# Performance work log

Hardware: AMD Instinct MI355X
Metric: run time of the kernel (lower is better)

## Reference

```python
import jax, jax.numpy as jnp
import numpy as np

N_HEAD = 16
LOCAL_CTX = 256
W_SCALE = 0.02  # keep logits in a sane range, like trained-net init


def setup_inputs() -> dict:
    key = jax.random.key(0)
    k1, k2, k3 = jax.random.split(key, 3)
    B, T, C = 4, 2048, 1024
    x = jax.random.normal(k1, (B, T, C), dtype=jnp.float32)
    W_attn = jax.random.normal(k2, (C, 3 * C), dtype=jnp.float32) * W_SCALE
    b_attn = jnp.zeros((3 * C,), dtype=jnp.float32)
    W_proj = jax.random.normal(k3, (C, C), dtype=jnp.float32) * W_SCALE
    b_proj = jnp.zeros((C,), dtype=jnp.float32)
    return {"x": x, "W_attn": W_attn, "b_attn": b_attn,
            "W_proj": W_proj, "b_proj": b_proj}


def _local_causal_mask(T, ctx):
    # token i attends to j with j <= i and i - j < ctx  (band of width ctx)
    i = jnp.arange(T)[:, None]
    j = jnp.arange(T)[None, :]
    ctx = min(T, ctx)
    return (j <= i) & ((i - j) < ctx)  # [T, T] bool


def reference(x, W_attn, b_attn, W_proj, b_proj):
    B, T, C = x.shape
    H = N_HEAD
    D = C // H
    qkv = x @ W_attn + b_attn                       # [B, T, 3C]
    q, k, v = jnp.split(qkv, 3, axis=-1)
    q = q.reshape(B, T, H, D).transpose(0, 2, 1, 3)  # [B, H, T, D]
    k = k.reshape(B, T, H, D).transpose(0, 2, 1, 3)
    v = v.reshape(B, T, H, D).transpose(0, 2, 1, 3)
    scale = 1.0 / jnp.sqrt(jnp.asarray(D, dtype=x.dtype))
    w = jnp.einsum('bhtd,bhsd->bhts', q, k) * scale  # [B, H, T, T]
    mask = _local_causal_mask(T, LOCAL_CTX)          # [T, T]
    w = jnp.where(mask[None, None], w, -jnp.inf)
    p = jax.nn.softmax(w, axis=-1)
    a = jnp.einsum('bhts,bhsd->bhtd', p, v)          # [B, H, T, D]
    y = a.transpose(0, 2, 1, 3).reshape(B, T, C)
    return y @ W_proj + b_proj
```

## Files before the change

kernel.cpp:

```cpp
#include <hip/hip_runtime.h>
#include <stdint.h>

#define B_SZ 4
#define T_SEQ 2048
#define C_DIM 1024
#define NH 16
#define DH 64
#define CTX 256

#define AS_G const __attribute__((address_space(1))) void*
#define AS_L __attribute__((address_space(3))) void*

typedef __attribute__((ext_vector_type(8))) short bf16x8;
typedef __attribute__((ext_vector_type(8))) unsigned short u16x8;
typedef __attribute__((ext_vector_type(4))) unsigned short u16x4;
typedef __attribute__((ext_vector_type(2))) unsigned int u32x2;
typedef __attribute__((ext_vector_type(4))) unsigned int u32x4;
typedef __attribute__((ext_vector_type(4))) float f32x4;

__device__ __forceinline__ float bf2f(unsigned short u) {
  unsigned int x = ((unsigned int)u) << 16;
  return __builtin_bit_cast(float, x);
}
__device__ __forceinline__ unsigned short f2bf(float f) {
  unsigned int u = __builtin_bit_cast(unsigned int, f);
  u = (u + 0x7FFFu + ((u >> 16) & 1u)) >> 16;
  return (unsigned short)u;
}
__device__ __forceinline__ unsigned int cvtpk(float lo, float hi) {
  unsigned int r;
  asm("v_cvt_pk_bf16_f32 %0, %1, %2" : "=v"(r) : "v"(lo), "v"(hi));
  return r;
}


__global__ void cvt_f32_bf16(const float* __restrict__ in,
                             unsigned short* __restrict__ out, int n8) {
  int i = blockIdx.x * blockDim.x + threadIdx.x;
  int stride = gridDim.x * blockDim.x;
  for (; i < n8; i += stride) {
    float4 a = ((const float4*)in)[2 * (size_t)i];
    float4 b = ((const float4*)in)[2 * (size_t)i + 1];
    u32x4 r;
    r[0] = cvtpk(a.x, a.y); r[1] = cvtpk(a.z, a.w);
    r[2] = cvtpk(b.x, b.y); r[3] = cvtpk(b.z, b.w);
    *(u32x4*)(out + 8 * (size_t)i) = r;
  }
}

__global__ void transpose_cvt(const float* __restrict__ W,
                              unsigned short* __restrict__ Wt, int R, int CC) {
  __shared__ float tile[32][33];
  int ct = blockIdx.x, rt = blockIdx.y;
  int tx = threadIdx.x & 31, ty = threadIdx.x >> 5;
#pragma unroll
  for (int i = 0; i < 4; ++i) {
    int r = ty + i * 8;
    tile[r][tx] = W[(size_t)(rt * 32 + r) * CC + ct * 32 + tx];
  }
  __syncthreads();
#pragma unroll
  for (int i = 0; i < 4; ++i) {
    int r = ty + i * 8;
    Wt[(size_t)(ct * 32 + r) * R + rt * 32 + tx] = f2bf(tile[tx][r]);
  }
}

#define BM 128
#define BN 128
#define BK 64

__global__ __launch_bounds__(256) void gemm_bt(
    const unsigned short* __restrict__ A, const unsigned short* __restrict__ Bt,
    const float* __restrict__ bias, int N, int K, int mode,
    float* __restrict__ outF, unsigned short* __restrict__ Qb,
    unsigned short* __restrict__ Kb, unsigned short* __restrict__ VTb) {
  __shared__ unsigned short As[BM * BK];
  __shared__ unsigned short Bs[BN * BK];
  const int tid = threadIdx.x;
  const int lane = tid & 63;
  const int w = tid >> 6;
  const int wm = w >> 1, wn = w & 1;

  const int nx = gridDim.x;
  int flat = blockIdx.y * nx + blockIdx.x;
  const int cpx = (nx * gridDim.y) >> 3;
  flat = (flat & 7) * cpx + (flat >> 3);
  const int m0 = (flat / nx) * BM, n0 = (flat % nx) * BN;

  const int srow = lane >> 3;
  const int sgch = (lane & 7) ^ srow;

  f32x4 acc[4][4];
#pragma unroll
  for (int mi = 0; mi < 4; ++mi)
#pragma unroll
    for (int ni = 0; ni < 4; ++ni) acc[mi][ni] = (f32x4){0.f, 0.f, 0.f, 0.f};

  for (int k0 = 0; k0 < K; k0 += BK) {
#pragma unroll
    for (int i = 0; i < 4; ++i) {
      int r8 = w * 4 + i;
      int row = r8 * 8 + srow;
      __builtin_amdgcn_global_load_lds(
          (AS_G)&A[(size_t)(m0 + row) * K + k0 + sgch * 8],
          (AS_L)((__attribute__((address_space(3))) unsigned short*)As + r8 * 512),
          16, 0, 0);
      __builtin_amdgcn_global_load_lds(
          (AS_G)&Bt[(size_t)(n0 + row) * K + k0 + sgch * 8],
          (AS_L)((__attribute__((address_space(3))) unsigned short*)Bs + r8 * 512),
          16, 0, 0);
    }
    __syncthreads();
#pragma unroll
    for (int ks = 0; ks < 2; ++ks) {
      bf16x8 av[4], bv[4];
      const int colc = (ks << 2) + (lane >> 4);
#pragma unroll
      for (int mi = 0; mi < 4; ++mi) {
        int row = wm * 64 + mi * 16 + (lane & 15);
        av[mi] = *(const bf16x8*)&As[row * BK + ((colc ^ (row & 7)) << 3)];
      }
#pragma unroll
      for (int ni = 0; ni < 4; ++ni) {
        int row = wn * 64 + ni * 16 + (lane & 15);
        bv[ni] = *(const bf16x8*)&Bs[row * BK + ((colc ^ (row & 7)) << 3)];
      }
#pragma unroll
      for (int mi = 0; mi < 4; ++mi)
#pragma unroll
        for (int ni = 0; ni < 4; ++ni)
          acc[mi][ni] = __builtin_amdgcn_mfma_f32_16x16x32_bf16(
              av[mi], bv[ni], acc[mi][ni], 0, 0, 0);
    }
    __syncthreads();
  }

#pragma unroll
  for (int mi = 0; mi < 4; ++mi) {
#pragma unroll
    for (int ni = 0; ni < 4; ++ni) {
      int gn = n0 + wn * 64 + ni * 16 + (lane & 15);
      float bb = bias[gn];
      int gmb = m0 + wm * 64 + mi * 16 + ((lane >> 4) << 2);
      if (mode == 0) {
#pragma unroll
        for (int j = 0; j < 4; ++j)
          outF[(size_t)(gmb + j) * N + gn] = acc[mi][ni][j] + bb;
      } else {
        int sec = gn >> 10, cc = gn & 1023;
        int h = cc >> 6, d = cc & 63;
        int b = gmb >> 11, t = gmb & 2047;
        if (sec == 2) {
          u32x2 pk;
          pk[0] = cvtpk(acc[mi][ni][0] + bb, acc[mi][ni][1] + bb);
          pk[1] = cvtpk(acc[mi][ni][2] + bb, acc[mi][ni][3] + bb);
          *(u32x2*)&VTb[((size_t)(b * NH + h) * DH + d) * T_SEQ + t] = pk;
        } else {
          size_t dst = (((size_t)(b * NH + h) * T_SEQ) + t) * DH + d;
          float sc = (sec == 0) ? 0.125f : 1.0f;
          float bbs = bb * sc;
          unsigned short* P = (sec == 0) ? Qb : Kb;
          unsigned int a = cvtpk(fmaf(acc[mi][ni][0], sc, bbs),
                                 fmaf(acc[mi][ni][1], sc, bbs));
          unsigned int c = cvtpk(fmaf(acc[mi][ni][2], sc, bbs),
                                 fmaf(acc[mi][ni][3], sc, bbs));
          P[dst] = (unsigned short)a;
          P[dst + DH] = (unsigned short)(a >> 16);
          P[dst + 2 * DH] = (unsigned short)c;
          P[dst + 3 * DH] = (unsigned short)(c >> 16);
        }
      }
    }
  }
}

__global__ __launch_bounds__(512, 4) void attn_mfma(
    const unsigned short* __restrict__ Qb,
    const unsigned short* __restrict__ Kb,
    const unsigned short* __restrict__ VT,
    unsigned short* __restrict__ Ab) {
  __shared__ unsigned short Ks[2][64 * 64];
  __shared__ unsigned short Vs[2][64 * 64];
  __shared__ unsigned short Pb[8][16][40];
  const int tid = threadIdx.x;
  const int w = tid >> 6, lane = tid & 63;
  const int lo = lane & 15, hi = lane >> 4;
  const int bh = blockIdx.x >> 4;
  const int t0 = (blockIdx.x & 15) * 128;
  const int b = bh >> 4, h = bh & 15;
  const size_t base = (size_t)bh * (T_SEQ * DH);
  const int t0w = t0 + 16 * w;
  const int tq = t0w + lo;
  const int sw = lo & 7;

  const int srow = tid >> 3;
  const int sgch = (tid & 7) ^ (srow & 7);

  const unsigned short* qp = Qb + base + (size_t)tq * DH + hi * 8;
  bf16x8 qa0 = *(const bf16x8*)qp;
  bf16x8 qa1 = *(const bf16x8*)(qp + 32);

  f32x4 O[4];
#pragma unroll
  for (int f = 0; f < 4; ++f) O[f] = (f32x4){0.f, 0.f, 0.f, 0.f};
  float lsum = 0.f;

  int kb_start = t0 - 256;
  if (kb_start < 0) kb_start = 0;
  const int kb_end = t0 + 128;
  const int nch = (kb_end - kb_start) >> 6;

  auto STAGE = [&](int kb, int bi) {
    __builtin_amdgcn_global_load_lds(
        (AS_G)&Kb[base + (size_t)(kb + srow) * DH + sgch * 8],
        (AS_L)((__attribute__((address_space(3))) unsigned short*)Ks[bi] +
               w * 512),
        16, 0, 0);
    __builtin_amdgcn_global_load_lds(
        (AS_G)&VT[base + (size_t)srow * T_SEQ + kb + sgch * 8],
        (AS_L)((__attribute__((address_space(3))) unsigned short*)Vs[bi] +
               w * 512),
        16, 0, 0);
  };

  STAGE(kb_start, 0);

  for (int ci = 0; ci < nch; ++ci) {
    const int kb = kb_start + (ci << 6);
    const int cb = ci & 1;
    const int kbn = (ci + 1 < nch) ? kb + 64 : kb;
    STAGE(kbn, cb ^ 1);
    asm volatile("s_waitcnt vmcnt(2)" ::: "memory");
    __builtin_amdgcn_sched_barrier(0);
    __builtin_amdgcn_s_barrier();
    __builtin_amdgcn_sched_barrier(0);

#pragma unroll
    for (int sb = 0; sb < 2; ++sb) {
      const int kbs = kb + 32 * sb;
      if (kbs > t0w + 15 || kbs + 31 < t0w - 255) continue;

      const int r0 = 32 * sb + lo, r1 = r0 + 16;
      bf16x8 kc0a = *(const bf16x8*)&Ks[cb][r0 * 64 + ((hi ^ sw) << 3)];
      bf16x8 kc0b = *(const bf16x8*)&Ks[cb][r0 * 64 + (((hi + 4) ^ sw) << 3)];
      bf16x8 kc1a = *(const bf16x8*)&Ks[cb][r1 * 64 + ((hi ^ sw) << 3)];
      bf16x8 kc1b = *(const bf16x8*)&Ks[cb][r1 * 64 + (((hi + 4) ^ sw) << 3)];

      __builtin_amdgcn_s_setprio(1);
      f32x4 s0 = __builtin_amdgcn_mfma_f32_16x16x32_bf16(
          kc0a, qa0, (f32x4){0.f, 0.f, 0.f, 0.f}, 0, 0, 0);
      s0 = __builtin_amdgcn_mfma_f32_16x16x32_bf16(kc0b, qa1, s0, 0, 0, 0);
      f32x4 s1 = __builtin_amdgcn_mfma_f32_16x16x32_bf16(
          kc1a, qa0, (f32x4){0.f, 0.f, 0.f, 0.f}, 0, 0, 0);
      s1 = __builtin_amdgcn_mfma_f32_16x16x32_bf16(kc1b, qa1, s1, 0, 0, 0);
      __builtin_amdgcn_s_setprio(0);

      float p[8];
      const bool full = (kbs >= t0w - 240) && (kbs + 31 <= t0w);
      if (full) {
#pragma unroll
        for (int j = 0; j < 4; ++j) {
          p[j] = __expf(s0[j]);
          p[4 + j] = __expf(s1[j]);
        }
      } else {
#pragma unroll
        for (int j = 0; j < 4; ++j) {
          int key = kbs + 4 * hi + j;
          p[j] = ((unsigned)(tq - key) < 256u) ? __expf(s0[j]) : 0.f;
          p[4 + j] = ((unsigned)(tq - key - 16) < 256u) ? __expf(s1[j]) : 0.f;
        }
      }
      lsum += ((p[0] + p[1]) + (p[2] + p[3])) + ((p[4] + p[5]) + (p[6] + p[7]));

      u32x2 w0, w1;
      w0[0] = cvtpk(p[0], p[1]); w0[1] = cvtpk(p[2], p[3]);
      w1[0] = cvtpk(p[4], p[5]); w1[1] = cvtpk(p[6], p[7]);
      *(u32x2*)&Pb[w][lo][4 * hi] = w0;
      *(u32x2*)&Pb[w][lo][16 + 4 * hi] = w1;

      bf16x8 pa = *(const bf16x8*)&Pb[w][lo][hi * 8];
      __builtin_amdgcn_s_setprio(1);
#pragma unroll
      for (int dt = 0; dt < 4; ++dt) {
        int vd = dt * 16 + lo;
        bf16x8 vf =
            *(const bf16x8*)&Vs[cb][vd * 64 + (((sb * 4 + hi) ^ sw) << 3)];
        O[dt] = __builtin_amdgcn_mfma_f32_16x16x32_bf16(vf, pa, O[dt], 0, 0, 0);
      }
      __builtin_amdgcn_s_setprio(0);
    }
    __builtin_amdgcn_s_barrier();
    __builtin_amdgcn_sched_barrier(0);
  }

  lsum += __shfl_xor(lsum, 16);
  lsum += __shfl_xor(lsum, 32);
  float inv = 1.f / lsum;
  size_t ob = ((size_t)(b * T_SEQ + tq)) * C_DIM + h * DH + 4 * hi;
#pragma unroll
  for (int dt = 0; dt < 4; ++dt) {
    u32x2 o;
    o[0] = cvtpk(O[dt][0] * inv, O[dt][1] * inv);
    o[1] = cvtpk(O[dt][2] * inv, O[dt][3] * inv);
    *(u32x2*)&Ab[ob + dt * 16] = o;
  }
}


extern "C" void kernel_launch(void* const* d_in, const int* in_sizes, int n_in,
                              void* d_out, int out_size, void* d_ws, size_t ws_size,
                              hipStream_t stream) {
  const float* x = (const float*)d_in[0];
  const float* Wa = (const float*)d_in[1];
  const float* ba = (const float*)d_in[2];
  const float* Wp = (const float*)d_in[3];
  const float* bp = (const float*)d_in[4];
  float* out = (float*)d_out;
  char* ws = (char*)d_ws;

  unsigned short* xb  = (unsigned short*)(ws);
  unsigned short* WaT = (unsigned short*)(ws + (16u << 20));
  unsigned short* WpT = (unsigned short*)(ws + (22u << 20));
  unsigned short* Qb  = (unsigned short*)(ws + (24u << 20));
  unsigned short* Kb  = (unsigned short*)(ws + (40u << 20));
  unsigned short* VT  = (unsigned short*)(ws + (56u << 20));
  unsigned short* Ab  = xb;

  cvt_f32_bf16<<<2048, 256, 0, stream>>>(x, xb, (B_SZ * T_SEQ * C_DIM) / 8);
  transpose_cvt<<<dim3(96, 32), 256, 0, stream>>>(Wa, WaT, C_DIM, 3 * C_DIM);
  transpose_cvt<<<dim3(32, 32), 256, 0, stream>>>(Wp, WpT, C_DIM, C_DIM);
  gemm_bt<<<dim3(3 * C_DIM / BN, B_SZ * T_SEQ / BM), 256, 0, stream>>>(
      xb, WaT, ba, 3 * C_DIM, C_DIM, 1, nullptr, Qb, Kb, VT);
  attn_mfma<<<B_SZ * NH * T_SEQ / 128, 512, 0, stream>>>(Qb, Kb, VT, Ab);
  gemm_bt<<<dim3(C_DIM / BN, B_SZ * T_SEQ / BM), 256, 0, stream>>>(
      Ab, WpT, bp, C_DIM, C_DIM, 0, out, nullptr, nullptr, nullptr);
}
```

Before: 135.8 us.

## Process two query tiles per attention block and drop GEMM tile swizzle

The attention kernel now handles 256 queries per block: each wave owns two 16-row query groups (A and B, 128 apart) that share each staged K/V chunk. This cuts redundant K/V loads for the overlapping windows and halves the grid. The cost is more registers per wave, fewer blocks, and a per-wave Pb scratch buffer reused by both groups. Separately, the GEMM drops its XCD-aware block remapping and uses plain blockIdx ordering, which may hurt L2 locality.

```diff
diff --git a/kernel.cpp b/kernel.cpp
--- a/kernel.cpp
+++ b/kernel.cpp
@@ -81,12 +81,7 @@
   const int lane = tid & 63;
   const int w = tid >> 6;
   const int wm = w >> 1, wn = w & 1;
-
-  const int nx = gridDim.x;
-  int flat = blockIdx.y * nx + blockIdx.x;
-  const int cpx = (nx * gridDim.y) >> 3;
-  flat = (flat & 7) * cpx + (flat >> 3);
-  const int m0 = (flat / nx) * BM, n0 = (flat % nx) * BN;
+  const int m0 = blockIdx.y * BM, n0 = blockIdx.x * BN;
 
   const int srow = lane >> 3;
   const int sgch = (lane & 7) ^ srow;
@@ -186,29 +181,36 @@
   const int tid = threadIdx.x;
   const int w = tid >> 6, lane = tid & 63;
   const int lo = lane & 15, hi = lane >> 4;
-  const int bh = blockIdx.x >> 4;
-  const int t0 = (blockIdx.x & 15) * 128;
+  const int bh = blockIdx.x >> 3;
+  const int t0 = (blockIdx.x & 7) * 256;
   const int b = bh >> 4, h = bh & 15;
   const size_t base = (size_t)bh * (T_SEQ * DH);
-  const int t0w = t0 + 16 * w;
-  const int tq = t0w + lo;
+  const int tA = t0 + 16 * w;
+  const int tB = tA + 128;
+  const int tqA = tA + lo, tqB = tB + lo;
   const int sw = lo & 7;
 
   const int srow = tid >> 3;
   const int sgch = (tid & 7) ^ (srow & 7);
 
-  const unsigned short* qp = Qb + base + (size_t)tq * DH + hi * 8;
-  bf16x8 qa0 = *(const bf16x8*)qp;
-  bf16x8 qa1 = *(const bf16x8*)(qp + 32);
-
-  f32x4 O[4];
-#pragma unroll
-  for (int f = 0; f < 4; ++f) O[f] = (f32x4){0.f, 0.f, 0.f, 0.f};
-  float lsum = 0.f;
+  const unsigned short* qpA = Qb + base + (size_t)tqA * DH + hi * 8;
+  bf16x8 qaA0 = *(const bf16x8*)qpA;
+  bf16x8 qaA1 = *(const bf16x8*)(qpA + 32);
+  const unsigned short* qpB = Qb + base + (size_t)tqB * DH + hi * 8;
+  bf16x8 qaB0 = *(const bf16x8*)qpB;
+  bf16x8 qaB1 = *(const bf16x8*)(qpB + 32);
+
+  f32x4 OA[4], OB[4];
+#pragma unroll
+  for (int f = 0; f < 4; ++f) {
+    OA[f] = (f32x4){0.f, 0.f, 0.f, 0.f};
+    OB[f] = (f32x4){0.f, 0.f, 0.f, 0.f};
+  }
+  float lsumA = 0.f, lsumB = 0.f;
 
   int kb_start = t0 - 256;
   if (kb_start < 0) kb_start = 0;
-  const int kb_end = t0 + 128;
+  const int kb_end = t0 + 256;
   const int nch = (kb_end - kb_start) >> 6;
 
   auto STAGE = [&](int kb, int bi) {
@@ -239,7 +241,9 @@
 #pragma unroll
     for (int sb = 0; sb < 2; ++sb) {
       const int kbs = kb + 32 * sb;
-      if (kbs > t0w + 15 || kbs + 31 < t0w - 255) continue;
+      const bool inA = !(kbs > tA + 15 || kbs + 31 < tA - 255);
+      const bool inB = !(kbs > tB + 15 || kbs + 31 < tB - 255);
+      if (!inA && !inB) continue;
 
       const int r0 = 32 * sb + lo, r1 = r0 + 16;
       bf16x8 kc0a = *(const bf16x8*)&Ks[cb][r0 * 64 + ((hi ^ sw) << 3)];
@@ -247,47 +251,84 @@
       bf16x8 kc1a = *(const bf16x8*)&Ks[cb][r1 * 64 + ((hi ^ sw) << 3)];
       bf16x8 kc1b = *(const bf16x8*)&Ks[cb][r1 * 64 + (((hi + 4) ^ sw) << 3)];
 
-      __builtin_amdgcn_s_setprio(1);
-      f32x4 s0 = __builtin_amdgcn_mfma_f32_16x16x32_bf16(
-          kc0a, qa0, (f32x4){0.f, 0.f, 0.f, 0.f}, 0, 0, 0);
-      s0 = __builtin_amdgcn_mfma_f32_16x16x32_bf16(kc0b, qa1, s0, 0, 0, 0);
-      f32x4 s1 = __builtin_amdgcn_mfma_f32_16x16x32_bf16(
-          kc1a, qa0, (f32x4){0.f, 0.f, 0.f, 0.f}, 0, 0, 0);
-      s1 = __builtin_amdgcn_mfma_f32_16x16x32_bf16(kc1b, qa1, s1, 0, 0, 0);
-      __builtin_amdgcn_s_setprio(0);
-
-      float p[8];
-      const bool full = (kbs >= t0w - 240) && (kbs + 31 <= t0w);
-      if (full) {
-#pragma unroll
-        for (int j = 0; j < 4; ++j) {
-          p[j] = __expf(s0[j]);
-          p[4 + j] = __expf(s1[j]);
+      bf16x8 paA, paB;
+      if (inA) {
+        __builtin_amdgcn_s_setprio(1);
+        f32x4 s0 = __builtin_amdgcn_mfma_f32_16x16x32_bf16(
+            kc0a, qaA0, (f32x4){0.f, 0.f, 0.f, 0.f}, 0, 0, 0);
+        s0 = __builtin_amdgcn_mfma_f32_16x16x32_bf16(kc0b, qaA1, s0, 0, 0, 0);
+        f32x4 s1 = __builtin_amdgcn_mfma_f32_16x16x32_bf16(
+            kc1a, qaA0, (f32x4){0.f, 0.f, 0.f, 0.f}, 0, 0, 0);
+        s1 = __builtin_amdgcn_mfma_f32_16x16x32_bf16(kc1b, qaA1, s1, 0, 0, 0);
+        __builtin_amdgcn_s_setprio(0);
+        float p[8];
+        const bool full = (kbs >= tA - 240) && (kbs + 31 <= tA);
+        if (full) {
+#pragma unroll
+          for (int j = 0; j < 4; ++j) {
+            p[j] = __expf(s0[j]);
+            p[4 + j] = __expf(s1[j]);
+          }
+        } else {
+#pragma unroll
+          for (int j = 0; j < 4; ++j) {
+            int key = kbs + 4 * hi + j;
+            p[j] = ((unsigned)(tqA - key) < 256u) ? __expf(s0[j]) : 0.f;
+            p[4 + j] = ((unsigned)(tqA - key - 16) < 256u) ? __expf(s1[j]) : 0.f;
+          }
         }
-      } else {
-#pragma unroll
-        for (int j = 0; j < 4; ++j) {
-          int key = kbs + 4 * hi + j;
-          p[j] = ((unsigned)(tq - key) < 256u) ? __expf(s0[j]) : 0.f;
-          p[4 + j] = ((unsigned)(tq - key - 16) < 256u) ? __expf(s1[j]) : 0.f;
+        lsumA += ((p[0] + p[1]) + (p[2] + p[3])) + ((p[4] + p[5]) + (p[6] + p[7]));
+        u32x2 w0, w1;
+        w0[0] = cvtpk(p[0], p[1]); w0[1] = cvtpk(p[2], p[3]);
+        w1[0] = cvtpk(p[4], p[5]); w1[1] = cvtpk(p[6], p[7]);
+        *(u32x2*)&Pb[w][lo][4 * hi] = w0;
+        *(u32x2*)&Pb[w][lo][16 + 4 * hi] = w1;
+        paA = *(const bf16x8*)&Pb[w][lo][hi * 8];
+      }
+      if (inB) {
+        __builtin_amdgcn_s_setprio(1);
+        f32x4 s0 = __builtin_amdgcn_mfma_f32_16x16x32_bf16(
+            kc0a, qaB0, (f32x4){0.f, 0.f, 0.f, 0.f}, 0, 0, 0);
+        s0 = __builtin_amdgcn_mfma_f32_16x16x32_bf16(kc0b, qaB1, s0, 0, 0, 0);
+        f32x4 s1 = __builtin_amdgcn_mfma_f32_16x16x32_bf16(
+            kc1a, qaB0, (f32x4){0.f, 0.f, 0.f, 0.f}, 0, 0, 0);
+        s1 = __builtin_amdgcn_mfma_f32_16x16x32_bf16(kc1b, qaB1, s1, 0, 0, 0);
+        __builtin_amdgcn_s_setprio(0);
+        float p[8];
+        const bool full = (kbs >= tB - 240) && (kbs + 31 <= tB);
+        if (full) {
+#pragma unroll
+          for (int j = 0; j < 4; ++j) {
+            p[j] = __expf(s0[j]);
+            p[4 + j] = __expf(s1[j]);
+          }
+        } else {
+#pragma unroll
+          for (int j = 0; j < 4; ++j) {
+            int key = kbs + 4 * hi + j;
+            p[j] = ((unsigned)(tqB - key) < 256u) ? __expf(s0[j]) : 0.f;
+            p[4 + j] = ((unsigned)(tqB - key - 16) < 256u) ? __expf(s1[j]) : 0.f;
+          }
         }
-      }
-      lsum += ((p[0] + p[1]) + (p[2] + p[3])) + ((p[4] + p[5]) + (p[6] + p[7]));
-
-      u32x2 w0, w1;
-      w0[0] = cvtpk(p[0], p[1]); w0[1] = cvtpk(p[2], p[3]);
-      w1[0] = cvtpk(p[4], p[5]); w1[1] = cvtpk(p[6], p[7]);
-      *(u32x2*)&Pb[w][lo][4 * hi] = w0;
-      *(u32x2*)&Pb[w][lo][16 + 4 * hi] = w1;
-
-      bf16x8 pa = *(const bf16x8*)&Pb[w][lo][hi * 8];
+        lsumB += ((p[0] + p[1]) + (p[2] + p[3])) + ((p[4] + p[5]) + (p[6] + p[7]));
+        u32x2 w0, w1;
+        w0[0] = cvtpk(p[0], p[1]); w0[1] = cvtpk(p[2], p[3]);
+        w1[0] = cvtpk(p[4], p[5]); w1[1] = cvtpk(p[6], p[7]);
+        *(u32x2*)&Pb[w][lo][4 * hi] = w0;
+        *(u32x2*)&Pb[w][lo][16 + 4 * hi] = w1;
+        paB = *(const bf16x8*)&Pb[w][lo][hi * 8];
+      }
+
       __builtin_amdgcn_s_setprio(1);
 #pragma unroll
       for (int dt = 0; dt < 4; ++dt) {
         int vd = dt * 16 + lo;
         bf16x8 vf =
             *(const bf16x8*)&Vs[cb][vd * 64 + (((sb * 4 + hi) ^ sw) << 3)];
-        O[dt] = __builtin_amdgcn_mfma_f32_16x16x32_bf16(vf, pa, O[dt], 0, 0, 0);
+        if (inA)
+          OA[dt] = __builtin_amdgcn_mfma_f32_16x16x32_bf16(vf, paA, OA[dt], 0, 0, 0);
+        if (inB)
+          OB[dt] = __builtin_amdgcn_mfma_f32_16x16x32_bf16(vf, paB, OB[dt], 0, 0, 0);
       }
       __builtin_amdgcn_s_setprio(0);
     }
@@ -295,16 +336,23 @@
     __builtin_amdgcn_sched_barrier(0);
   }
 
-  lsum += __shfl_xor(lsum, 16);
-  lsum += __shfl_xor(lsum, 32);
-  float inv = 1.f / lsum;
-  size_t ob = ((size_t)(b * T_SEQ + tq)) * C_DIM + h * DH + 4 * hi;
+  lsumA += __shfl_xor(lsumA, 16);
+  lsumA += __shfl_xor(lsumA, 32);
+  lsumB += __shfl_xor(lsumB, 16);
+  lsumB += __shfl_xor(lsumB, 32);
+  float invA = 1.f / lsumA, invB = 1.f / lsumB;
+  size_t obA = ((size_t)(b * T_SEQ + tqA)) * C_DIM + h * DH + 4 * hi;
+  size_t obB = ((size_t)(b * T_SEQ + tqB)) * C_DIM + h * DH + 4 * hi;
 #pragma unroll
   for (int dt = 0; dt < 4; ++dt) {
     u32x2 o;
-    o[0] = cvtpk(O[dt][0] * inv, O[dt][1] * inv);
-    o[1] = cvtpk(O[dt][2] * inv, O[dt][3] * inv);
-    *(u32x2*)&Ab[ob + dt * 16] = o;
+    o[0] = cvtpk(OA[dt][0] * invA, OA[dt][1] * invA);
+    o[1] = cvtpk(OA[dt][2] * invA, OA[dt][3] * invA);
+    *(u32x2*)&Ab[obA + dt * 16] = o;
+    u32x2 o2;
+    o2[0] = cvtpk(OB[dt][0] * invB, OB[dt][1] * invB);
+    o2[1] = cvtpk(OB[dt][2] * invB, OB[dt][3] * invB);
+    *(u32x2*)&Ab[obB + dt * 16] = o2;
   }
 }
 
@@ -333,7 +381,7 @@
   transpose_cvt<<<dim3(32, 32), 256, 0, stream>>>(Wp, WpT, C_DIM, C_DIM);
   gemm_bt<<<dim3(3 * C_DIM / BN, B_SZ * T_SEQ / BM), 256, 0, stream>>>(
       xb, WaT, ba, 3 * C_DIM, C_DIM, 1, nullptr, Qb, Kb, VT);
-  attn_mfma<<<B_SZ * NH * T_SEQ / 128, 512, 0, stream>>>(Qb, Kb, VT, Ab);
+  attn_mfma<<<B_SZ * NH * T_SEQ / 256, 512, 0, stream>>>(Qb, Kb, VT, Ab);
   gemm_bt<<<dim3(C_DIM / BN, B_SZ * T_SEQ / BM), 256, 0, stream>>>(
       Ab, WpT, bp, C_DIM, C_DIM, 0, out, nullptr, nullptr, nullptr);
 }
```

New measurement: 137.3 us. About the same (+1.1%).

## Double-buffer GEMM LDS tiles and prefetch next K-slice during MFMA

Applied to the files above, without the earlier changes.

The GEMM now keeps two LDS buffers for the A and B tiles and issues the global-to-LDS loads for the next K slice before computing on the current one, waiting with a partial vmcnt. This overlaps memory traffic with MFMA work instead of serialising them. It also adds s_setprio around the MFMA block and drops the grouped block-index swizzle in favour of plain row-major tile mapping, which may reduce L2 reuse. LDS use doubles, which can lower occupancy.

```diff
diff --git a/kernel.cpp b/kernel.cpp
--- a/kernel.cpp
+++ b/kernel.cpp
@@ -75,18 +75,13 @@
     const float* __restrict__ bias, int N, int K, int mode,
     float* __restrict__ outF, unsigned short* __restrict__ Qb,
     unsigned short* __restrict__ Kb, unsigned short* __restrict__ VTb) {
-  __shared__ unsigned short As[BM * BK];
-  __shared__ unsigned short Bs[BN * BK];
+  __shared__ unsigned short As[2][BM * BK];
+  __shared__ unsigned short Bs[2][BN * BK];
   const int tid = threadIdx.x;
   const int lane = tid & 63;
   const int w = tid >> 6;
   const int wm = w >> 1, wn = w & 1;
-
-  const int nx = gridDim.x;
-  int flat = blockIdx.y * nx + blockIdx.x;
-  const int cpx = (nx * gridDim.y) >> 3;
-  flat = (flat & 7) * cpx + (flat >> 3);
-  const int m0 = (flat / nx) * BM, n0 = (flat % nx) * BN;
+  const int m0 = blockIdx.y * BM, n0 = blockIdx.x * BN;
 
   const int srow = lane >> 3;
   const int sgch = (lane & 7) ^ srow;
@@ -97,21 +92,37 @@
 #pragma unroll
     for (int ni = 0; ni < 4; ++ni) acc[mi][ni] = (f32x4){0.f, 0.f, 0.f, 0.f};
 
-  for (int k0 = 0; k0 < K; k0 += BK) {
+  const int nk = K / BK;
+
+  auto STAGE = [&](int k0, int bi) {
 #pragma unroll
     for (int i = 0; i < 4; ++i) {
       int r8 = w * 4 + i;
       int row = r8 * 8 + srow;
       __builtin_amdgcn_global_load_lds(
           (AS_G)&A[(size_t)(m0 + row) * K + k0 + sgch * 8],
-          (AS_L)((__attribute__((address_space(3))) unsigned short*)As + r8 * 512),
+          (AS_L)((__attribute__((address_space(3))) unsigned short*)As[bi] +
+                 r8 * 512),
           16, 0, 0);
       __builtin_amdgcn_global_load_lds(
           (AS_G)&Bt[(size_t)(n0 + row) * K + k0 + sgch * 8],
-          (AS_L)((__attribute__((address_space(3))) unsigned short*)Bs + r8 * 512),
+          (AS_L)((__attribute__((address_space(3))) unsigned short*)Bs[bi] +
+                 r8 * 512),
           16, 0, 0);
     }
-    __syncthreads();
+  };
+
+  STAGE(0, 0);
+
+  for (int ki = 0; ki < nk; ++ki) {
+    const int cb = ki & 1;
+    const int kn = (ki + 1 < nk) ? (ki + 1) * BK : ki * BK;
+    STAGE(kn, cb ^ 1);
+    asm volatile("s_waitcnt vmcnt(8)" ::: "memory");
+    __builtin_amdgcn_sched_barrier(0);
+    __builtin_amdgcn_s_barrier();
+    __builtin_amdgcn_sched_barrier(0);
+
 #pragma unroll
     for (int ks = 0; ks < 2; ++ks) {
       bf16x8 av[4], bv[4];
@@ -119,21 +130,24 @@
 #pragma unroll
       for (int mi = 0; mi < 4; ++mi) {
         int row = wm * 64 + mi * 16 + (lane & 15);
-        av[mi] = *(const bf16x8*)&As[row * BK + ((colc ^ (row & 7)) << 3)];
+        av[mi] = *(const bf16x8*)&As[cb][row * BK + ((colc ^ (row & 7)) << 3)];
       }
 #pragma unroll
       for (int ni = 0; ni < 4; ++ni) {
         int row = wn * 64 + ni * 16 + (lane & 15);
-        bv[ni] = *(const bf16x8*)&Bs[row * BK + ((colc ^ (row & 7)) << 3)];
-      }
+        bv[ni] = *(const bf16x8*)&Bs[cb][row * BK + ((colc ^ (row & 7)) << 3)];
+      }
+      __builtin_amdgcn_s_setprio(1);
 #pragma unroll
       for (int mi = 0; mi < 4; ++mi)
 #pragma unroll
         for (int ni = 0; ni < 4; ++ni)
           acc[mi][ni] = __builtin_amdgcn_mfma_f32_16x16x32_bf16(
               av[mi], bv[ni], acc[mi][ni], 0, 0, 0);
+      __builtin_amdgcn_s_setprio(0);
     }
-    __syncthreads();
+    __builtin_amdgcn_s_barrier();
+    __builtin_amdgcn_sched_barrier(0);
   }
 
 #pragma unroll
```

Result: slower. 139.4 us (+2.7%).
